# Optimization experiments

Measured on AMD Instinct MI355X. Metric: run time of the kernel, lower is better.

Reference implementation:

```python
import jax, jax.numpy as jnp
import numpy as np

B, M, N, D, H = 4, 8, 128, 32, 64
SMALL_V = 1e-8


def setup_inputs() -> dict:
    key = jax.random.key(0)
    ks = jax.random.split(key, 12)
    s = 0.05
    x = jax.random.normal(ks[0], (B, M, N, D), jnp.float32)
    sizes = jax.random.randint(ks[1], (B,), N // 2, N + 1)
    valid = (jnp.arange(N)[None, :] < sizes[:, None]).astype(jnp.float32)  # [B,N]
    x = x * valid[:, None, :, None]  # zero out padded items
    return {
        "x": x,
        "x_size": sizes.astype(jnp.float32),
        "W1a": jax.random.normal(ks[2], (D, 2 * D), jnp.float32) * s,
        "b1a": jax.random.normal(ks[3], (2 * D,), jnp.float32) * s,
        "W1b": jax.random.normal(ks[4], (2 * D, D), jnp.float32) * s,
        "b1b": jax.random.normal(ks[5], (D,), jnp.float32) * s,
        "W2a": jax.random.normal(ks[6], (D, 2 * D), jnp.float32) * s,
        "b2a": jax.random.normal(ks[7], (2 * D,), jnp.float32) * s,
        "W2b": jax.random.normal(ks[8], (2 * D, H), jnp.float32) * s,
        "b2b": jax.random.normal(ks[9], (H,), jnp.float32) * s,
        "w3": jax.random.normal(ks[10], (H,), jnp.float32) * s,
        "b3": jax.random.normal(ks[11], (1,), jnp.float32) * s,
    }


def _item_mask(x):
    # 1.0 where the item's feature row has any nonzero entry, else 0.0. [...,N,1]
    return jnp.any(x != 0, axis=-1, keepdims=True).astype(x.dtype)


def _set_norm(x, x_size):
    # layer_normalization with is_set_norm=True: normalize over (N*D) per set,
    # dividing by the true valid size x_size*D and masking padded items.
    b, m, n, d = x.shape
    mask = jnp.broadcast_to(_item_mask(x), x.shape).reshape(b, m, n * d)
    xr = x.reshape(b, m, n * d)
    denom = x_size[:, None] * d  # [B,1] -> broadcasts over nSet
    mean = jnp.sum(xr, axis=-1) / denom  # [B,M]
    diff = xr - mean[..., None]
    std = jnp.sqrt(jnp.sum(diff * diff * mask, axis=-1) / denom)  # [B,M]
    out = diff / (std[..., None] + SMALL_V) * mask
    return out.reshape(b, m, n, d)


def reference(x, x_size, W1a, b1a, W1b, b1b, W2a, b2a, W2b, b2b, w3, b3):
    mask = _item_mask(x)  # [B,M,N,1]
    x_orig = x
    xn = _set_norm(x, x_size) * mask  # [B,M,N,D]
    # MLP1 (rank-4 -> masked by its own input's item mask)
    m1 = _item_mask(xn)
    x1 = (jnp.matmul(jax.nn.gelu(jnp.matmul(xn, W1a) + b1a), W1b) + b1b) * m1
    # pairwise differences: x_diff[b,m,i,j,:] = x1[b,m,i,:] - xn[b,m,j,:]
    x_diff = x1[:, :, :, None, :] - xn[:, :, None, :, :]  # [B,M,N,N,D]
    # MLP2 (rank-5 -> no mask, is_SoftMax=0)
    e = jnp.matmul(jax.nn.gelu(jnp.matmul(x_diff, W2a) + b2a), W2b) + b2b  # [B,M,N,N,H]
    # aggregation: out[b,m,j,h,d] = sum_i e[b,m,i,j,h] * x1[b,m,i,d]
    agg = jnp.einsum('bmijh,bmid->bmjhd', e, x1)
    # MLP3_linear: Dense(1) over H, then squeeze
    out = jnp.einsum('bmjhd,h->bmjd', agg, w3) + b3[0]
    out = (out + x_orig) * mask
    return out
```

## Files before the change

kernel.cpp:

```cpp
#include <hip/hip_runtime.h>

#define NNC 128
#define DDC 32
#define KKC 64
constexpr int ND = NNC * DDC;
#define SMALLV 1e-8f

__device__ __forceinline__ float gelu_f(float v) {
    float v2 = v * v;
    float p  = fmaf(0.1029432f, v2, 2.3022082f);
    float e  = __builtin_amdgcn_exp2f(v * p);
    float r  = __builtin_amdgcn_rcpf(e + 1.0f);
    return fmaf(-v, r, v);
}

__global__ __launch_bounds__(256, 1) void fused2(
    const float* __restrict__ x, const float* __restrict__ x_size,
    const float* __restrict__ W1a, const float* __restrict__ b1a,
    const float* __restrict__ W1b, const float* __restrict__ b1b,
    const float* __restrict__ W2a, const float* __restrict__ b2a,
    const float* __restrict__ W2b, const float* __restrict__ b2b,
    const float* __restrict__ w3, const float* __restrict__ b3,
    float* __restrict__ out)
{
    __shared__ __align__(16) float smem[16384];

    const int t   = threadIdx.x;
    const int blk = blockIdx.x;
    const int bm  = blk >> 3;
    const int jt  = blk & 7;
    const int k   = t & 63;
    const int w   = t >> 6;
    const int dL  = t & 31;

    const int iN = (int)(x_size[bm >> 3] + 0.5f);

    float* sX1  = smem;
    float* sA1  = smem + 4096;
    float* sXn  = smem + 4096;
    float* sH32 = smem + 8192;
    float* scr  = smem + 8192;
    float* sA2  = smem + 12416;
    float* sS   = smem + 13568;
    float* sV2  = smem + 15872;
    float* sAny = smem + 15936;
    float* sRed = smem + 16064;
    float* sC3  = smem + 16072;

    if (jt * 16 >= iN) {
        ((float2*)(out + (size_t)bm * ND + jt * 512))[t] = make_float2(0.f, 0.f);
        return;
    }

    float colA[32];
    #pragma unroll
    for (int d = 0; d < 32; ++d) colA[d] = W1a[d * 64 + k];
    float colB[64];
    #pragma unroll
    for (int q = 0; q < 64; ++q) colB[q] = W1b[q * 32 + dL];
    const float rb1a = b1a[k];
    const float rb1b = b1b[dL];
    const float rb2a = b2a[k];

    {
        const int kk = t >> 2, hq = t & 3;
        float p = 0.f;
        #pragma unroll
        for (int h = 0; h < 16; ++h)
            p = fmaf(W2b[kk * 64 + hq * 16 + h], w3[hq * 16 + h], p);
        scr[t] = p;
    }
    if (t < 64) {
        float q = b2b[t] * w3[t];
        #pragma unroll
        for (int off = 32; off; off >>= 1) q += __shfl_xor(q, off);
        if (t == 0) sC3[0] = q;
    }
    if (t < 128) sAny[t] = 0.f;
    __syncthreads();

    const float4* xs4 = (const float4*)(x + (size_t)bm * ND);
    float4 v4[4];
    float lsum = 0.f;
    #pragma unroll
    for (int s = 0; s < 4; ++s) {
        int f = t + s * 256;
        float4 q = xs4[f];
        v4[s] = q;
        lsum += q.x + q.y + q.z + q.w;
        if (q.x != 0.f || q.y != 0.f || q.z != 0.f || q.w != 0.f) sAny[f >> 3] = 1.f;
    }
    #pragma unroll
    for (int off = 32; off; off >>= 1) lsum += __shfl_xor(lsum, off);
    if ((t & 63) == 0) sRed[w] = lsum;
    __syncthreads();
    if ((t & 3) == 0)
        sV2[t >> 2] = scr[t] + scr[t + 1] + scr[t + 2] + scr[t + 3];
    const float denom = x_size[bm >> 3] * 32.f;
    const float mean  = (sRed[0] + sRed[1] + sRed[2] + sRed[3]) / denom;
    float lsq = 0.f;
    #pragma unroll
    for (int s = 0; s < 4; ++s) {
        int f = t + s * 256;
        float mk = sAny[f >> 3];
        float dx = v4[s].x - mean, dy = v4[s].y - mean;
        float dz = v4[s].z - mean, dw = v4[s].w - mean;
        lsq += mk * (dx * dx + dy * dy + dz * dz + dw * dw);
    }
    #pragma unroll
    for (int off = 32; off; off >>= 1) lsq += __shfl_xor(lsq, off);
    __syncthreads();
    if ((t & 63) == 0) sRed[w] = lsq;
    __syncthreads();
    const float sq  = sRed[0] + sRed[1] + sRed[2] + sRed[3];
    const float inv = 1.f / (sqrtf(sq / denom) + SMALLV);

    #pragma unroll
    for (int s = 0; s < 4; ++s) {
        int f = t + s * 256;
        float mk = sAny[f >> 3] * inv;
        float4 q = v4[s];
        q.x = (q.x - mean) * mk; q.y = (q.y - mean) * mk;
        q.z = (q.z - mean) * mk; q.w = (q.w - mean) * mk;
        ((float4*)sXn)[f] = q;
    }
    __syncthreads();

    for (int c = 0; c < 4; ++c) {
        const int rb = c * 32;
        const bool live = (rb < iN);
        if (live) {
            #pragma unroll
            for (int r = 0; r < 8; ++r) {
                const int nl = w + 4 * r;
                const float4* xr4 = (const float4*)&sXn[(rb + nl) * 32];
                float acc = rb1a;
                #pragma unroll
                for (int dq = 0; dq < 8; ++dq) {
                    float4 xv = xr4[dq];
                    acc = fmaf(xv.x, colA[4 * dq + 0], acc);
                    acc = fmaf(xv.y, colA[4 * dq + 1], acc);
                    acc = fmaf(xv.z, colA[4 * dq + 2], acc);
                    acc = fmaf(xv.w, colA[4 * dq + 3], acc);
                }
                sH32[nl * 64 + k] = gelu_f(acc);
            }
        }
        __syncthreads();
        if (live) {
            #pragma unroll
            for (int p = 0; p < 4; ++p) {
                const int nl = (t >> 5) + 8 * p;
                const float4* hr4 = (const float4*)&sH32[nl * 64];
                float acc = rb1b;
                #pragma unroll
                for (int qq = 0; qq < 16; ++qq) {
                    float4 hv = hr4[qq];
                    acc = fmaf(hv.x, colB[4 * qq + 0], acc);
                    acc = fmaf(hv.y, colB[4 * qq + 1], acc);
                    acc = fmaf(hv.z, colB[4 * qq + 2], acc);
                    acc = fmaf(hv.w, colB[4 * qq + 3], acc);
                }
                sX1[(rb + nl) * 32 + dL] = acc * sAny[rb + nl];
            }
        } else {
            #pragma unroll
            for (int p = 0; p < 4; ++p)
                sX1[(rb + (t >> 5) + 8 * p) * 32 + dL] = 0.f;
        }
        __syncthreads();
    }

    float colC[32];
    #pragma unroll
    for (int d = 0; d < 32; ++d) colC[d] = W2a[d * 64 + k];
    #pragma unroll
    for (int q = 0; q < 4; ++q) {
        const int jl = w + 4 * q;
        const float4* xr4 = (const float4*)&sXn[(jt * 16 + jl) * 32];
        float acc = 0.f;
        #pragma unroll
        for (int dq = 0; dq < 8; ++dq) {
            float4 xv = xr4[dq];
            acc = fmaf(xv.x, colC[4 * dq + 0], acc);
            acc = fmaf(xv.y, colC[4 * dq + 1], acc);
            acc = fmaf(xv.z, colC[4 * dq + 2], acc);
            acc = fmaf(xv.w, colC[4 * dq + 3], acc);
        }
        sA2[k * 18 + jl] = acc;
    }
    __syncthreads();

    const int ICAP = (iN + 3) & ~3;
    for (int n = w; n < ICAP; n += 4) {
        const float4* x14 = (const float4*)&sX1[n * 32];
        float acc = rb2a;
        #pragma unroll
        for (int dq = 0; dq < 8; ++dq) {
            float4 xv = x14[dq];
            acc = fmaf(xv.x, colC[4 * dq + 0], acc);
            acc = fmaf(xv.y, colC[4 * dq + 1], acc);
            acc = fmaf(xv.z, colC[4 * dq + 2], acc);
            acc = fmaf(xv.w, colC[4 * dq + 3], acc);
        }
        sA1[n * 65 + k] = acc;
    }
    __syncthreads();

    const float c3 = sC3[0];
    {
        const int jp = t & 7;
        const int ic = t >> 3;
        const int i0 = ic * 4;
        if (i0 < iN) {
            float a0x = c3, a0y = c3, a1x = c3, a1y = c3;
            float a2x = c3, a2y = c3, a3x = c3, a3y = c3;
            #pragma unroll 4
            for (int kk = 0; kk < 64; ++kk) {
                const float2 a2v = *(const float2*)&sA2[kk * 18 + 2 * jp];
                const float vk  = sV2[kk];
                const float* a1p = &sA1[i0 * 65 + kk];
                const float b0 = a1p[0];
                const float b1 = a1p[65];
                const float b2 = a1p[130];
                const float b3r = a1p[195];
                a0x = fmaf(gelu_f(b0 - a2v.x), vk, a0x);
                a0y = fmaf(gelu_f(b0 - a2v.y), vk, a0y);
                a1x = fmaf(gelu_f(b1 - a2v.x), vk, a1x);
                a1y = fmaf(gelu_f(b1 - a2v.y), vk, a1y);
                a2x = fmaf(gelu_f(b2 - a2v.x), vk, a2x);
                a2y = fmaf(gelu_f(b2 - a2v.y), vk, a2y);
                a3x = fmaf(gelu_f(b3r - a2v.x), vk, a3x);
                a3y = fmaf(gelu_f(b3r - a2v.y), vk, a3y);
            }
            *(float2*)&sS[(i0 + 0) * 18 + 2 * jp] = make_float2(a0x, a0y);
            *(float2*)&sS[(i0 + 1) * 18 + 2 * jp] = make_float2(a1x, a1y);
            *(float2*)&sS[(i0 + 2) * 18 + 2 * jp] = make_float2(a2x, a2y);
            *(float2*)&sS[(i0 + 3) * 18 + 2 * jp] = make_float2(a3x, a3y);
        }
    }
    __syncthreads();

    {
        const int j  = t >> 4;
        const int d0 = (t & 15) * 2;
        const int jg = jt * 16 + j;
        float s0 = 0.f, s1 = 0.f;
        #pragma unroll 4
        for (int i = 0; i < ICAP; ++i) {
            const float Sv = sS[i * 18 + j];
            const float2 xv = *(const float2*)&sX1[i * 32 + d0];
            s0 = fmaf(Sv, xv.x, s0);
            s1 = fmaf(Sv, xv.y, s1);
        }
        const float msk = sAny[jg];
        const float b3v = b3[0];
        const size_t ob = (size_t)bm * ND + jg * 32 + d0;
        const float2 xo = *(const float2*)&x[ob];
        float2 o;
        o.x = (s0 + b3v + xo.x) * msk;
        o.y = (s1 + b3v + xo.y) * msk;
        *(float2*)&out[ob] = o;
    }
}

extern "C" void kernel_launch(void* const* d_in, const int* in_sizes, int n_in,
                              void* d_out, int out_size, void* d_ws, size_t ws_size,
                              hipStream_t stream) {
    (void)in_sizes; (void)n_in; (void)d_ws; (void)ws_size; (void)out_size;
    const float* x      = (const float*)d_in[0];
    const float* x_size = (const float*)d_in[1];
    const float* W1a    = (const float*)d_in[2];
    const float* b1a    = (const float*)d_in[3];
    const float* W1b    = (const float*)d_in[4];
    const float* b1b    = (const float*)d_in[5];
    const float* W2a    = (const float*)d_in[6];
    const float* b2a    = (const float*)d_in[7];
    const float* W2b    = (const float*)d_in[8];
    const float* b2b    = (const float*)d_in[9];
    const float* w3     = (const float*)d_in[10];
    const float* b3     = (const float*)d_in[11];
    float* out = (float*)d_out;

    fused2<<<dim3(256), dim3(256), 0, stream>>>(
        x, x_size, W1a, b1a, W1b, b1b, W2a, b2a, W2b, b2b, w3, b3, out);
}
```

Before: 106.9 us.

## Double block size to 512 threads and transpose pairwise-stage smem layouts

Raises the thread count per block from 256 to 512 and redistributes every stage (normalization, MLP1, A1/A2 projections, pairwise GELU reduction, aggregation) across the doubled threads. The pairwise stage now gives each thread one j and four i values, reading float4-vectorized rows from transposed, 68-padded A1/A2 arrays. The aggregation stage uses a transposed S buffer for float4 loads. This is meant to raise latency hiding and cut LDS instruction count. In exchange, register pressure per thread rises under the 512-thread launch bound, and each thread does less work to amortize its per-thread loads.

Result: faster. 99.42 us (-7.0%).

```diff
diff --git a/kernel.cpp b/kernel.cpp
--- a/kernel.cpp
+++ b/kernel.cpp
@@ -14,7 +14,7 @@
     return fmaf(-v, r, v);
 }
 
-__global__ __launch_bounds__(256, 1) void fused2(
+__global__ __launch_bounds__(512, 1) void fused3(
     const float* __restrict__ x, const float* __restrict__ x_size,
     const float* __restrict__ W1a, const float* __restrict__ b1a,
     const float* __restrict__ W1b, const float* __restrict__ b1b,
@@ -39,16 +39,16 @@
     float* sA1  = smem + 4096;
     float* sXn  = smem + 4096;
     float* sH32 = smem + 8192;
-    float* scr  = smem + 8192;
-    float* sA2  = smem + 12416;
-    float* sS   = smem + 13568;
-    float* sV2  = smem + 15872;
-    float* sAny = smem + 15936;
-    float* sRed = smem + 16064;
-    float* sC3  = smem + 16072;
+    float* scr  = smem + 12800;
+    float* sA2t = smem + 12800;
+    float* sSt  = smem + 13888;
+    float* sV2  = smem + 16000;
+    float* sAny = smem + 16064;
+    float* sRed = smem + 16192;
+    float* sC3  = smem + 16200;
 
     if (jt * 16 >= iN) {
-        ((float2*)(out + (size_t)bm * ND + jt * 512))[t] = make_float2(0.f, 0.f);
+        out[(size_t)bm * ND + jt * 512 + t] = 0.f;
         return;
     }
 
@@ -63,11 +63,11 @@
     const float rb2a = b2a[k];
 
     {
-        const int kk = t >> 2, hq = t & 3;
+        const int kk = t >> 3, hq = t & 7;
         float p = 0.f;
         #pragma unroll
-        for (int h = 0; h < 16; ++h)
-            p = fmaf(W2b[kk * 64 + hq * 16 + h], w3[hq * 16 + h], p);
+        for (int h = 0; h < 8; ++h)
+            p = fmaf(W2b[kk * 64 + hq * 8 + h], w3[hq * 8 + h], p);
         scr[t] = p;
     }
     if (t < 64) {
@@ -80,11 +80,11 @@
     __syncthreads();
 
     const float4* xs4 = (const float4*)(x + (size_t)bm * ND);
-    float4 v4[4];
+    float4 v4[2];
     float lsum = 0.f;
     #pragma unroll
-    for (int s = 0; s < 4; ++s) {
-        int f = t + s * 256;
+    for (int s = 0; s < 2; ++s) {
+        int f = t + s * 512;
         float4 q = xs4[f];
         v4[s] = q;
         lsum += q.x + q.y + q.z + q.w;
@@ -94,14 +94,22 @@
     for (int off = 32; off; off >>= 1) lsum += __shfl_xor(lsum, off);
     if ((t & 63) == 0) sRed[w] = lsum;
     __syncthreads();
-    if ((t & 3) == 0)
-        sV2[t >> 2] = scr[t] + scr[t + 1] + scr[t + 2] + scr[t + 3];
+    if (t < 64) {
+        float vp = 0.f;
+        #pragma unroll
+        for (int q = 0; q < 8; ++q) vp += scr[t * 8 + q];
+        sV2[t] = vp;
+    }
     const float denom = x_size[bm >> 3] * 32.f;
-    const float mean  = (sRed[0] + sRed[1] + sRed[2] + sRed[3]) / denom;
+    float mean = 0.f;
+    #pragma unroll
+    for (int r = 0; r < 8; ++r) mean += sRed[r];
+    mean /= denom;
+
     float lsq = 0.f;
     #pragma unroll
-    for (int s = 0; s < 4; ++s) {
-        int f = t + s * 256;
+    for (int s = 0; s < 2; ++s) {
+        int f = t + s * 512;
         float mk = sAny[f >> 3];
         float dx = v4[s].x - mean, dy = v4[s].y - mean;
         float dz = v4[s].z - mean, dw = v4[s].w - mean;
@@ -112,12 +120,14 @@
     __syncthreads();
     if ((t & 63) == 0) sRed[w] = lsq;
     __syncthreads();
-    const float sq  = sRed[0] + sRed[1] + sRed[2] + sRed[3];
+    float sq = 0.f;
+    #pragma unroll
+    for (int r = 0; r < 8; ++r) sq += sRed[r];
     const float inv = 1.f / (sqrtf(sq / denom) + SMALLV);
 
     #pragma unroll
-    for (int s = 0; s < 4; ++s) {
-        int f = t + s * 256;
+    for (int s = 0; s < 2; ++s) {
+        int f = t + s * 512;
         float mk = sAny[f >> 3] * inv;
         float4 q = v4[s];
         q.x = (q.x - mean) * mk; q.y = (q.y - mean) * mk;
@@ -131,8 +141,8 @@
         const bool live = (rb < iN);
         if (live) {
             #pragma unroll
-            for (int r = 0; r < 8; ++r) {
-                const int nl = w + 4 * r;
+            for (int r = 0; r < 4; ++r) {
+                const int nl = w + 8 * r;
                 const float4* xr4 = (const float4*)&sXn[(rb + nl) * 32];
                 float acc = rb1a;
                 #pragma unroll
@@ -149,8 +159,8 @@
         __syncthreads();
         if (live) {
             #pragma unroll
-            for (int p = 0; p < 4; ++p) {
-                const int nl = (t >> 5) + 8 * p;
+            for (int p = 0; p < 2; ++p) {
+                const int nl = (t >> 5) + 16 * p;
                 const float4* hr4 = (const float4*)&sH32[nl * 64];
                 float acc = rb1b;
                 #pragma unroll
@@ -165,8 +175,8 @@
             }
         } else {
             #pragma unroll
-            for (int p = 0; p < 4; ++p)
-                sX1[(rb + (t >> 5) + 8 * p) * 32 + dL] = 0.f;
+            for (int p = 0; p < 2; ++p)
+                sX1[(rb + (t >> 5) + 16 * p) * 32 + dL] = 0.f;
         }
         __syncthreads();
     }
@@ -175,8 +185,8 @@
     #pragma unroll
     for (int d = 0; d < 32; ++d) colC[d] = W2a[d * 64 + k];
     #pragma unroll
-    for (int q = 0; q < 4; ++q) {
-        const int jl = w + 4 * q;
+    for (int q = 0; q < 2; ++q) {
+        const int jl = w + 8 * q;
         const float4* xr4 = (const float4*)&sXn[(jt * 16 + jl) * 32];
         float acc = 0.f;
         #pragma unroll
@@ -187,12 +197,12 @@
             acc = fmaf(xv.z, colC[4 * dq + 2], acc);
             acc = fmaf(xv.w, colC[4 * dq + 3], acc);
         }
-        sA2[k * 18 + jl] = acc;
+        sA2t[jl * 68 + k] = acc;
     }
     __syncthreads();
 
     const int ICAP = (iN + 3) & ~3;
-    for (int n = w; n < ICAP; n += 4) {
+    for (int n = w; n < ICAP; n += 8) {
         const float4* x14 = (const float4*)&sX1[n * 32];
         float acc = rb2a;
         #pragma unroll
@@ -203,64 +213,67 @@
             acc = fmaf(xv.z, colC[4 * dq + 2], acc);
             acc = fmaf(xv.w, colC[4 * dq + 3], acc);
         }
-        sA1[n * 65 + k] = acc;
-    }
-    __syncthreads();
-
-    const float c3 = sC3[0];
+        sA1[n * 68 + k] = acc;
+    }
+    __syncthreads();
+
     {
-        const int jp = t & 7;
-        const int ic = t >> 3;
-        const int i0 = ic * 4;
+        const float c3 = sC3[0];
+        const int j  = t & 15;
+        const int i0 = (t >> 4) * 4;
         if (i0 < iN) {
-            float a0x = c3, a0y = c3, a1x = c3, a1y = c3;
-            float a2x = c3, a2y = c3, a3x = c3, a3y = c3;
+            float a0 = c3, a1 = c3, a2 = c3, a3 = c3;
+            const float* a2row = &sA2t[j * 68];
+            const float* b0r = &sA1[(i0 + 0) * 68];
+            const float* b1r = &sA1[(i0 + 1) * 68];
+            const float* b2r = &sA1[(i0 + 2) * 68];
+            const float* b3r = &sA1[(i0 + 3) * 68];
             #pragma unroll 4
-            for (int kk = 0; kk < 64; ++kk) {
-                const float2 a2v = *(const float2*)&sA2[kk * 18 + 2 * jp];
-                const float vk  = sV2[kk];
-                const float* a1p = &sA1[i0 * 65 + kk];
-                const float b0 = a1p[0];
-                const float b1 = a1p[65];
-                const float b2 = a1p[130];
-                const float b3r = a1p[195];
-                a0x = fmaf(gelu_f(b0 - a2v.x), vk, a0x);
-                a0y = fmaf(gelu_f(b0 - a2v.y), vk, a0y);
-                a1x = fmaf(gelu_f(b1 - a2v.x), vk, a1x);
-                a1y = fmaf(gelu_f(b1 - a2v.y), vk, a1y);
-                a2x = fmaf(gelu_f(b2 - a2v.x), vk, a2x);
-                a2y = fmaf(gelu_f(b2 - a2v.y), vk, a2y);
-                a3x = fmaf(gelu_f(b3r - a2v.x), vk, a3x);
-                a3y = fmaf(gelu_f(b3r - a2v.y), vk, a3y);
+            for (int kk = 0; kk < 64; kk += 4) {
+                float4 va = *(const float4*)&a2row[kk];
+                float4 vv = *(const float4*)&sV2[kk];
+                float4 q0 = *(const float4*)&b0r[kk];
+                float4 q1 = *(const float4*)&b1r[kk];
+                float4 q2 = *(const float4*)&b2r[kk];
+                float4 q3 = *(const float4*)&b3r[kk];
+                a0 = fmaf(gelu_f(q0.x - va.x), vv.x, a0);
+                a1 = fmaf(gelu_f(q1.x - va.x), vv.x, a1);
+                a2 = fmaf(gelu_f(q2.x - va.x), vv.x, a2);
+                a3 = fmaf(gelu_f(q3.x - va.x), vv.x, a3);
+                a0 = fmaf(gelu_f(q0.y - va.y), vv.y, a0);
+                a1 = fmaf(gelu_f(q1.y - va.y), vv.y, a1);
+                a2 = fmaf(gelu_f(q2.y - va.y), vv.y, a2);
+                a3 = fmaf(gelu_f(q3.y - va.y), vv.y, a3);
+                a0 = fmaf(gelu_f(q0.z - va.z), vv.z, a0);
+                a1 = fmaf(gelu_f(q1.z - va.z), vv.z, a1);
+                a2 = fmaf(gelu_f(q2.z - va.z), vv.z, a2);
+                a3 = fmaf(gelu_f(q3.z - va.z), vv.z, a3);
+                a0 = fmaf(gelu_f(q0.w - va.w), vv.w, a0);
+                a1 = fmaf(gelu_f(q1.w - va.w), vv.w, a1);
+                a2 = fmaf(gelu_f(q2.w - va.w), vv.w, a2);
+                a3 = fmaf(gelu_f(q3.w - va.w), vv.w, a3);
             }
-            *(float2*)&sS[(i0 + 0) * 18 + 2 * jp] = make_float2(a0x, a0y);
-            *(float2*)&sS[(i0 + 1) * 18 + 2 * jp] = make_float2(a1x, a1y);
-            *(float2*)&sS[(i0 + 2) * 18 + 2 * jp] = make_float2(a2x, a2y);
-            *(float2*)&sS[(i0 + 3) * 18 + 2 * jp] = make_float2(a3x, a3y);
+            *(float4*)&sSt[j * 132 + i0] = make_float4(a0, a1, a2, a3);
         }
     }
     __syncthreads();
 
     {
-        const int j  = t >> 4;
-        const int d0 = (t & 15) * 2;
-        const int jg = jt * 16 + j;
-        float s0 = 0.f, s1 = 0.f;
-        #pragma unroll 4
-        for (int i = 0; i < ICAP; ++i) {
-            const float Sv = sS[i * 18 + j];
-            const float2 xv = *(const float2*)&sX1[i * 32 + d0];
-            s0 = fmaf(Sv, xv.x, s0);
-            s1 = fmaf(Sv, xv.y, s1);
-        }
+        const int jA = t >> 5;
+        const int dA = t & 31;
+        const float* strow = &sSt[jA * 132];
+        float s0 = 0.f;
+        for (int i = 0; i < ICAP; i += 4) {
+            float4 sv = *(const float4*)&strow[i];
+            s0 = fmaf(sv.x, sX1[(i + 0) * 32 + dA], s0);
+            s0 = fmaf(sv.y, sX1[(i + 1) * 32 + dA], s0);
+            s0 = fmaf(sv.z, sX1[(i + 2) * 32 + dA], s0);
+            s0 = fmaf(sv.w, sX1[(i + 3) * 32 + dA], s0);
+        }
+        const int jg = jt * 16 + jA;
         const float msk = sAny[jg];
-        const float b3v = b3[0];
-        const size_t ob = (size_t)bm * ND + jg * 32 + d0;
-        const float2 xo = *(const float2*)&x[ob];
-        float2 o;
-        o.x = (s0 + b3v + xo.x) * msk;
-        o.y = (s1 + b3v + xo.y) * msk;
-        *(float2*)&out[ob] = o;
+        const size_t ob = (size_t)bm * ND + jg * 32 + dA;
+        out[ob] = (s0 + b3[0] + x[ob]) * msk;
     }
 }
 
@@ -282,6 +295,6 @@
     const float* b3     = (const float*)d_in[11];
     float* out = (float*)d_out;
 
-    fused2<<<dim3(256), dim3(256), 0, stream>>>(
+    fused3<<<dim3(256), dim3(512), 0, stream>>>(
         x, x_size, W1a, b1a, W1b, b1b, W2a, b2a, W2b, b2b, w3, b3, out);
 }
```
